# Kernel optimization log

Measured on AMD Instinct MI355X. Metric: run time of the kernel, lower is better.

Reference implementation:

```python
import jax, jax.numpy as jnp
import numpy as np

N_NODES = 50000
N_EDGES = 800000
D = 128          # in_feats == out_feats (residual connection)
E_DIMS = 128
NEG_SLOPE = 0.01  # F.leaky_relu default


def setup_inputs() -> dict:
    key = jax.random.key(0)
    ks = jax.random.split(key, 7)
    h = jax.random.normal(ks[0], (N_NODES, D), dtype=jnp.float32)
    edge_w = jax.random.normal(ks[1], (N_EDGES, E_DIMS), dtype=jnp.float32)
    W_self = jax.random.normal(ks[2], (D, D), dtype=jnp.float32) * (2.0 / D) ** 0.5
    W_func = jax.random.normal(ks[3], (D, D), dtype=jnp.float32) * (2.0 / D) ** 0.5
    W_att = jax.random.normal(ks[4], (1, 2 * D + E_DIMS), dtype=jnp.float32) * 0.1
    src = jax.random.randint(ks[5], (N_EDGES,), 0, N_NODES, dtype=jnp.int32)
    dst = jax.random.randint(ks[6], (N_EDGES,), 0, N_NODES, dtype=jnp.int32)
    return {"h": h, "edge_w": edge_w, "W_self": W_self, "W_func": W_func,
            "W_att": W_att, "src": src, "dst": dst}


def reference(h, edge_w, W_self, W_func, W_att, src, dst):
    N = h.shape[0]
    h_in = h
    h_s = h @ W_self.T                     # [N, D] self transform
    z = h @ W_func.T                       # [N, D] message transform

    # attention logit: leaky_relu(W_att @ [z_src, z_dst, e_w]) -- split the
    # single linear into per-node / per-edge pieces (same math, no big concat)
    wa = W_att[0]
    s_src = z @ wa[:D]                     # [N]
    s_dst = z @ wa[D:2 * D]                # [N]
    s_e = edge_w @ wa[2 * D:]              # [E]
    logits = jax.nn.leaky_relu(s_src[src] + s_dst[dst] + s_e, NEG_SLOPE)  # [E]

    # edge softmax grouped by destination node (ragged mailboxes)
    m = jax.ops.segment_max(logits, dst, num_segments=N)
    m = jnp.where(jnp.isfinite(m), m, 0.0)
    ex = jnp.exp(logits - m[dst])
    denom = jax.ops.segment_sum(ex, dst, num_segments=N)
    a = ex / jnp.maximum(denom[dst], 1e-9)                     # [E]

    # weighted scatter-sum of source messages
    agg = jax.ops.segment_sum(a[:, None] * z[src], dst, num_segments=N)  # [N, D]

    # DGL: nodes with zero in-degree keep their original ndata['h']
    deg = jax.ops.segment_sum(jnp.ones_like(logits), dst, num_segments=N)
    h_new = jnp.where(deg[:, None] > 0, h_s + agg, h_in)

    h_new = jax.nn.relu(h_new)             # relu=True
    return h_in + h_new                    # res_connection=True
```

## Files before the change

### kernel.cpp

```cpp
#include <hip/hip_runtime.h>
#include <math.h>

#define D 128
constexpr int NT = 64;
constexpr int CAP = 128;

static __device__ __forceinline__ unsigned bf16_rn(float x) {
    unsigned u = __float_as_uint(x);
    return (u + 0x7fffu + ((u >> 16) & 1u)) >> 16;
}
static __device__ __forceinline__ unsigned pack_bf16x2(float lo, float hi) {
    return bf16_rn(lo) | (bf16_rn(hi) << 16);
}
static __device__ __forceinline__ float2 unpack_bf16x2(unsigned u) {
    return make_float2(__uint_as_float(u << 16),
                       __uint_as_float(u & 0xffff0000u));
}

__global__ __launch_bounds__(256) void node_transform(
    const float* __restrict__ h, const float* __restrict__ Wf,
    const float* __restrict__ Ws, const float* __restrict__ wa,
    unsigned* __restrict__ zp, float* __restrict__ s_src,
    float* __restrict__ s_dst, float* __restrict__ hs_out, int N)
{
    __shared__ float tile[NT * D];
    const int t = threadIdx.x;
    const int n0 = blockIdx.x * NT;
    const int nvalid = min(NT, N - n0);

    {
        const float4* __restrict__ src4 = (const float4*)(h + (size_t)n0 * D);
        float4* dst4 = (float4*)tile;
        #pragma unroll
        for (int i = 0; i < 8; ++i) {
            int idx = t + i * 256;
            float4 v = make_float4(0.f, 0.f, 0.f, 0.f);
            if ((idx >> 5) < nvalid) v = src4[idx];
            dst4[idx] = v;
        }
    }
    __syncthreads();

    const int oi = t & 31;
    const int q  = t >> 5;
    const int rows[4] = { 2 * oi, 2 * oi + 1, 64 + 2 * oi, 64 + 2 * oi + 1 };

    float acc[8][4];

    #pragma unroll
    for (int n = 0; n < 8; ++n)
        #pragma unroll
        for (int m = 0; m < 4; ++m) acc[n][m] = 0.f;

    for (int kk = 0; kk < D; kk += 8) {
        float4 w[4][2];
        #pragma unroll
        for (int m = 0; m < 4; ++m) {
            const float* wr = Wf + (size_t)rows[m] * D + kk;
            w[m][0] = *(const float4*)wr;
            w[m][1] = *(const float4*)(wr + 4);
        }
        #pragma unroll
        for (int n = 0; n < 8; ++n) {
            const float* hp = &tile[(q * 8 + n) * D + kk];
            float4 a = *(const float4*)hp;
            float4 b = *(const float4*)(hp + 4);
            #pragma unroll
            for (int m = 0; m < 4; ++m) {
                acc[n][m] += a.x * w[m][0].x + a.y * w[m][0].y
                           + a.z * w[m][0].z + a.w * w[m][0].w
                           + b.x * w[m][1].x + b.y * w[m][1].y
                           + b.z * w[m][1].z + b.w * w[m][1].w;
            }
        }
    }

    {
        #pragma unroll
        for (int n = 0; n < 8; ++n) {
            int node = q * 8 + n;
            if (node < nvalid) {
                unsigned* op = zp + (size_t)(n0 + node) * 64;
                op[oi]      = pack_bf16x2(acc[n][0], acc[n][1]);
                op[32 + oi] = pack_bf16x2(acc[n][2], acc[n][3]);
            }
        }
        const float ws0 = wa[rows[0]],     ws1 = wa[rows[1]];
        const float ws2 = wa[rows[2]],     ws3 = wa[rows[3]];
        const float wd0 = wa[D + rows[0]], wd1 = wa[D + rows[1]];
        const float wd2 = wa[D + rows[2]], wd3 = wa[D + rows[3]];
        #pragma unroll
        for (int n = 0; n < 8; ++n) {
            float ps = acc[n][0] * ws0 + acc[n][1] * ws1
                     + acc[n][2] * ws2 + acc[n][3] * ws3;
            float pd = acc[n][0] * wd0 + acc[n][1] * wd1
                     + acc[n][2] * wd2 + acc[n][3] * wd3;
            #pragma unroll
            for (int off = 16; off > 0; off >>= 1) {
                ps += __shfl_xor(ps, off, 32);
                pd += __shfl_xor(pd, off, 32);
            }
            int node = q * 8 + n;
            if (oi == 0 && node < nvalid) {
                s_src[n0 + node] = ps;
                s_dst[n0 + node] = pd;
            }
        }
    }

    #pragma unroll
    for (int n = 0; n < 8; ++n)
        #pragma unroll
        for (int m = 0; m < 4; ++m) acc[n][m] = 0.f;

    for (int kk = 0; kk < D; kk += 8) {
        float4 w[4][2];
        #pragma unroll
        for (int m = 0; m < 4; ++m) {
            const float* wr = Ws + (size_t)rows[m] * D + kk;
            w[m][0] = *(const float4*)wr;
            w[m][1] = *(const float4*)(wr + 4);
        }
        #pragma unroll
        for (int n = 0; n < 8; ++n) {
            const float* hp = &tile[(q * 8 + n) * D + kk];
            float4 a = *(const float4*)hp;
            float4 b = *(const float4*)(hp + 4);
            #pragma unroll
            for (int m = 0; m < 4; ++m) {
                acc[n][m] += a.x * w[m][0].x + a.y * w[m][0].y
                           + a.z * w[m][0].z + a.w * w[m][0].w
                           + b.x * w[m][1].x + b.y * w[m][1].y
                           + b.z * w[m][1].z + b.w * w[m][1].w;
            }
        }
    }

    #pragma unroll
    for (int n = 0; n < 8; ++n) {
        int node = q * 8 + n;
        if (node < nvalid) {
            float* op = hs_out + (size_t)(n0 + node) * D;
            *(float2*)(op + 2 * oi)      = make_float2(acc[n][0], acc[n][1]);
            *(float2*)(op + 64 + 2 * oi) = make_float2(acc[n][2], acc[n][3]);
        }
    }
}

__global__ __launch_bounds__(256) void edge_score_scatter(
    const float* __restrict__ edge_w, const float* __restrict__ wa,
    const int* __restrict__ src, const int* __restrict__ dst,
    const float* __restrict__ s_src, const float* __restrict__ s_dst,
    int* __restrict__ cursor, int2* __restrict__ bkt, int E)
{
    const int lg = threadIdx.x & 15;
    const int g0 = (blockIdx.x * blockDim.x + threadIdx.x) >> 4;
    const int ng = (gridDim.x * blockDim.x) >> 4;
    const float4* wa4 = (const float4*)(wa + 2 * D);
    const float4 w0 = wa4[2 * lg];
    const float4 w1 = wa4[2 * lg + 1];
    for (int e = g0; e < E; e += ng) {
        const float4* ewp = (const float4*)(edge_w + (size_t)e * D);
        float4 a = ewp[2 * lg];
        float4 b = ewp[2 * lg + 1];
        float p = a.x * w0.x + a.y * w0.y + a.z * w0.z + a.w * w0.w
                + b.x * w1.x + b.y * w1.y + b.z * w1.z + b.w * w1.w;
        p += __shfl_xor(p, 1, 16);
        p += __shfl_xor(p, 2, 16);
        p += __shfl_xor(p, 4, 16);
        p += __shfl_xor(p, 8, 16);
        if (lg == 0) {
            int s = src[e];
            int d = dst[e];
            float logit = s_src[s] + s_dst[d] + p;
            logit = (logit > 0.f) ? logit : 0.01f * logit;
            float ex = __expf(logit);
            int rank = atomicAdd(cursor + d, 1);
            if (rank < CAP)
                bkt[((size_t)d << 7) + rank] = make_int2(s, __float_as_int(ex));
        }
    }
}

__global__ __launch_bounds__(256) void agg_finalize(
    const int* __restrict__ cursor, const int2* __restrict__ bkt,
    const unsigned* __restrict__ zp, const float* __restrict__ h,
    const float* __restrict__ h_s, float* __restrict__ out, int N)
{
    const int lane = threadIdx.x & 63;
    const int n = blockIdx.x * 4 + (threadIdx.x >> 6);
    if (n >= N) return;
    const size_t b = (size_t)n << 7;
    const int dg = min(cursor[n], CAP);
    float ax = 0.f, ay = 0.f, dsum = 0.f;
    int e = 0;
    for (; e + 8 <= dg; e += 8) {
        int2 p[8];
        #pragma unroll
        for (int j = 0; j < 8; ++j) p[j] = bkt[b + e + j];
        unsigned zv[8];
        #pragma unroll
        for (int j = 0; j < 8; ++j)
            zv[j] = zp[(size_t)p[j].x * 64 + lane];
        #pragma unroll
        for (int j = 0; j < 8; ++j) {
            float ex = __int_as_float(p[j].y);
            float2 z2 = unpack_bf16x2(zv[j]);
            dsum += ex;
            ax += ex * z2.x;
            ay += ex * z2.y;
        }
    }
    if (e + 4 <= dg) {
        int2 p[4];
        #pragma unroll
        for (int j = 0; j < 4; ++j) p[j] = bkt[b + e + j];
        unsigned zv[4];
        #pragma unroll
        for (int j = 0; j < 4; ++j)
            zv[j] = zp[(size_t)p[j].x * 64 + lane];
        #pragma unroll
        for (int j = 0; j < 4; ++j) {
            float ex = __int_as_float(p[j].y);
            float2 z2 = unpack_bf16x2(zv[j]);
            dsum += ex;
            ax += ex * z2.x;
            ay += ex * z2.y;
        }
        e += 4;
    }
    for (; e < dg; ++e) {
        int2 p = bkt[b + e];
        float ex = __int_as_float(p.y);
        float2 z2 = unpack_bf16x2(zp[(size_t)p.x * 64 + lane]);
        dsum += ex;
        ax += ex * z2.x;
        ay += ex * z2.y;
    }
    float2 hv = *(const float2*)(h + (size_t)n * D + 2 * lane);
    float rx, ry;
    if (dg > 0) {
        float inv = 1.f / fmaxf(dsum, 1e-9f);
        float2 hs = *(const float2*)(h_s + (size_t)n * D + 2 * lane);
        rx = hs.x + ax * inv;
        ry = hs.y + ay * inv;
    } else {
        rx = hv.x; ry = hv.y;
    }
    rx = fmaxf(rx, 0.f); ry = fmaxf(ry, 0.f);
    float2 o = make_float2(hv.x + rx, hv.y + ry);
    *(float2*)(out + (size_t)n * D + 2 * lane) = o;
}

extern "C" void kernel_launch(void* const* d_in, const int* in_sizes, int n_in,
                              void* d_out, int out_size, void* d_ws, size_t ws_size,
                              hipStream_t stream)
{
    const float* h      = (const float*)d_in[0];
    const float* edge_w = (const float*)d_in[1];
    const float* W_self = (const float*)d_in[2];
    const float* W_func = (const float*)d_in[3];
    const float* W_att  = (const float*)d_in[4];
    const int*   src    = (const int*)d_in[5];
    const int*   dst    = (const int*)d_in[6];
    float* out = (float*)d_out;

    const int N = in_sizes[0] / D;
    const int E = in_sizes[1] / D;

    unsigned* zp  = (unsigned*)d_ws;
    float* s_src  = (float*)(zp + (size_t)N * 64);
    float* s_dst  = s_src + N;
    int*   cursor = (int*)(s_dst + N);
    int2*  bkt    = (int2*)(cursor + N);

    hipMemsetAsync(cursor, 0, (size_t)N * sizeof(int), stream);

    node_transform<<<(N + NT - 1) / NT, 256, 0, stream>>>(
        h, W_func, W_self, W_att, zp, s_src, s_dst, out, N);

    edge_score_scatter<<<2048, 256, 0, stream>>>(edge_w, W_att, src, dst,
                                                 s_src, s_dst, cursor, bkt, E);

    agg_finalize<<<(N + 3) / 4, 256, 0, stream>>>(cursor, bkt, zp, h, out, out, N);
}
```

Before: 753.0 us.

## Fuse node transform and edge scoring into one launch, defer softmax to aggregation

The edge-scoring pass now has no dependence on the node transform: it stores only the raw edge-feature score in the bucket, and the node-side s_src/s_dst terms, leaky-relu and exp move into the aggregation kernel. That lets the node-transform blocks and the edge-scatter blocks share a single launch with a block-index split, so the memory-bound edge_w stream overlaps the GEMM work and one launch boundary disappears. In exchange, aggregation does an extra gather of s_src per edge plus the exp, and the fused kernel's edge blocks carry the shared-memory tile reservation, which may lower their occupancy.

```diff
diff --git a/kernel.cpp b/kernel.cpp
--- a/kernel.cpp
+++ b/kernel.cpp
@@ -3,6 +3,7 @@
 
 #define D 128
 constexpr int NT = 64;
+constexpr int EB = 2048;
 constexpr int CAP = 128;
 
 static __device__ __forceinline__ unsigned bf16_rn(float x) {
@@ -17,14 +18,46 @@
                        __uint_as_float(u & 0xffff0000u));
 }
 
-__global__ __launch_bounds__(256) void node_transform(
+__global__ __launch_bounds__(256) void fused_transform_edge(
     const float* __restrict__ h, const float* __restrict__ Wf,
     const float* __restrict__ Ws, const float* __restrict__ wa,
-    unsigned* __restrict__ zp, float* __restrict__ s_src,
-    float* __restrict__ s_dst, float* __restrict__ hs_out, int N)
+    const float* __restrict__ edge_w, const int* __restrict__ src,
+    const int* __restrict__ dst, unsigned* __restrict__ zp,
+    float* __restrict__ s_src, float* __restrict__ s_dst,
+    float* __restrict__ hs_out, int* __restrict__ cursor,
+    int2* __restrict__ bkt, int N, int E, int NBK1)
 {
     __shared__ float tile[NT * D];
     const int t = threadIdx.x;
+
+    if ((int)blockIdx.x >= NBK1) {
+        const int lg = t & 15;
+        const int g0 = (((int)blockIdx.x - NBK1) * 256 + t) >> 4;
+        const int ng = (EB * 256) >> 4;
+        const float4* wa4 = (const float4*)(wa + 2 * D);
+        const float4 w0 = wa4[2 * lg];
+        const float4 w1 = wa4[2 * lg + 1];
+        for (int e = g0; e < E; e += ng) {
+            const float4* ewp = (const float4*)(edge_w + (size_t)e * D);
+            float4 a = ewp[2 * lg];
+            float4 b = ewp[2 * lg + 1];
+            float p = a.x * w0.x + a.y * w0.y + a.z * w0.z + a.w * w0.w
+                    + b.x * w1.x + b.y * w1.y + b.z * w1.z + b.w * w1.w;
+            p += __shfl_xor(p, 1, 16);
+            p += __shfl_xor(p, 2, 16);
+            p += __shfl_xor(p, 4, 16);
+            p += __shfl_xor(p, 8, 16);
+            if (lg == 0) {
+                int d = dst[e];
+                int rank = atomicAdd(cursor + d, 1);
+                if (rank < CAP)
+                    bkt[((size_t)d << 7) + rank] =
+                        make_int2(src[e], __float_as_int(p));
+            }
+        }
+        return;
+    }
+
     const int n0 = blockIdx.x * NT;
     const int nvalid = min(NT, N - n0);
 
@@ -147,44 +180,10 @@
     }
 }
 
-__global__ __launch_bounds__(256) void edge_score_scatter(
-    const float* __restrict__ edge_w, const float* __restrict__ wa,
-    const int* __restrict__ src, const int* __restrict__ dst,
-    const float* __restrict__ s_src, const float* __restrict__ s_dst,
-    int* __restrict__ cursor, int2* __restrict__ bkt, int E)
-{
-    const int lg = threadIdx.x & 15;
-    const int g0 = (blockIdx.x * blockDim.x + threadIdx.x) >> 4;
-    const int ng = (gridDim.x * blockDim.x) >> 4;
-    const float4* wa4 = (const float4*)(wa + 2 * D);
-    const float4 w0 = wa4[2 * lg];
-    const float4 w1 = wa4[2 * lg + 1];
-    for (int e = g0; e < E; e += ng) {
-        const float4* ewp = (const float4*)(edge_w + (size_t)e * D);
-        float4 a = ewp[2 * lg];
-        float4 b = ewp[2 * lg + 1];
-        float p = a.x * w0.x + a.y * w0.y + a.z * w0.z + a.w * w0.w
-                + b.x * w1.x + b.y * w1.y + b.z * w1.z + b.w * w1.w;
-        p += __shfl_xor(p, 1, 16);
-        p += __shfl_xor(p, 2, 16);
-        p += __shfl_xor(p, 4, 16);
-        p += __shfl_xor(p, 8, 16);
-        if (lg == 0) {
-            int s = src[e];
-            int d = dst[e];
-            float logit = s_src[s] + s_dst[d] + p;
-            logit = (logit > 0.f) ? logit : 0.01f * logit;
-            float ex = __expf(logit);
-            int rank = atomicAdd(cursor + d, 1);
-            if (rank < CAP)
-                bkt[((size_t)d << 7) + rank] = make_int2(s, __float_as_int(ex));
-        }
-    }
-}
-
 __global__ __launch_bounds__(256) void agg_finalize(
     const int* __restrict__ cursor, const int2* __restrict__ bkt,
-    const unsigned* __restrict__ zp, const float* __restrict__ h,
+    const unsigned* __restrict__ zp, const float* __restrict__ s_src,
+    const float* __restrict__ s_dst, const float* __restrict__ h,
     const float* __restrict__ h_s, float* __restrict__ out, int N)
 {
     const int lane = threadIdx.x & 63;
@@ -192,6 +191,7 @@
     if (n >= N) return;
     const size_t b = (size_t)n << 7;
     const int dg = min(cursor[n], CAP);
+    const float sdn = s_dst[n];
     float ax = 0.f, ay = 0.f, dsum = 0.f;
     int e = 0;
     for (; e + 8 <= dg; e += 8) {
@@ -199,12 +199,17 @@
         #pragma unroll
         for (int j = 0; j < 8; ++j) p[j] = bkt[b + e + j];
         unsigned zv[8];
-        #pragma unroll
-        for (int j = 0; j < 8; ++j)
+        float ss[8];
+        #pragma unroll
+        for (int j = 0; j < 8; ++j) {
             zv[j] = zp[(size_t)p[j].x * 64 + lane];
+            ss[j] = s_src[p[j].x];
+        }
         #pragma unroll
         for (int j = 0; j < 8; ++j) {
-            float ex = __int_as_float(p[j].y);
+            float logit = ss[j] + sdn + __int_as_float(p[j].y);
+            logit = (logit > 0.f) ? logit : 0.01f * logit;
+            float ex = __expf(logit);
             float2 z2 = unpack_bf16x2(zv[j]);
             dsum += ex;
             ax += ex * z2.x;
@@ -216,12 +221,17 @@
         #pragma unroll
         for (int j = 0; j < 4; ++j) p[j] = bkt[b + e + j];
         unsigned zv[4];
-        #pragma unroll
-        for (int j = 0; j < 4; ++j)
+        float ss[4];
+        #pragma unroll
+        for (int j = 0; j < 4; ++j) {
             zv[j] = zp[(size_t)p[j].x * 64 + lane];
+            ss[j] = s_src[p[j].x];
+        }
         #pragma unroll
         for (int j = 0; j < 4; ++j) {
-            float ex = __int_as_float(p[j].y);
+            float logit = ss[j] + sdn + __int_as_float(p[j].y);
+            logit = (logit > 0.f) ? logit : 0.01f * logit;
+            float ex = __expf(logit);
             float2 z2 = unpack_bf16x2(zv[j]);
             dsum += ex;
             ax += ex * z2.x;
@@ -231,7 +241,9 @@
     }
     for (; e < dg; ++e) {
         int2 p = bkt[b + e];
-        float ex = __int_as_float(p.y);
+        float logit = s_src[p.x] + sdn + __int_as_float(p.y);
+        logit = (logit > 0.f) ? logit : 0.01f * logit;
+        float ex = __expf(logit);
         float2 z2 = unpack_bf16x2(zp[(size_t)p.x * 64 + lane]);
         dsum += ex;
         ax += ex * z2.x;
@@ -267,6 +279,7 @@
 
     const int N = in_sizes[0] / D;
     const int E = in_sizes[1] / D;
+    const int NBK1 = (N + NT - 1) / NT;
 
     unsigned* zp  = (unsigned*)d_ws;
     float* s_src  = (float*)(zp + (size_t)N * 64);
@@ -276,11 +289,10 @@
 
     hipMemsetAsync(cursor, 0, (size_t)N * sizeof(int), stream);
 
-    node_transform<<<(N + NT - 1) / NT, 256, 0, stream>>>(
-        h, W_func, W_self, W_att, zp, s_src, s_dst, out, N);
-
-    edge_score_scatter<<<2048, 256, 0, stream>>>(edge_w, W_att, src, dst,
-                                                 s_src, s_dst, cursor, bkt, E);
-
-    agg_finalize<<<(N + 3) / 4, 256, 0, stream>>>(cursor, bkt, zp, h, out, out, N);
-}
+    fused_transform_edge<<<NBK1 + EB, 256, 0, stream>>>(
+        h, W_func, W_self, W_att, edge_w, src, dst,
+        zp, s_src, s_dst, out, cursor, bkt, N, E, NBK1);
+
+    agg_finalize<<<(N + 3) / 4, 256, 0, stream>>>(cursor, bkt, zp, s_src, s_dst,
+                                                  h, out, out, N);
+}
```

After: 764.8 us. No clear change (+1.6%).
